# Kernel tuning notes

Hardware: AMD Instinct MI355X
Metric: run time of the kernel (lower is better)

The kernel has to match this reference:

```python
import jax, jax.numpy as jnp
import numpy as np

NODE_DIM = 256
HID = 128        # out_channels per head
HEADS = 4
NLAYERS = 2
OUT_DIM = 128
LM, LT = 30, 50
N = LM + LT       # 80 nodes per duplex graph
F = HID * HEADS   # 512
B = 1024
LN_EPS = 1e-5

def _build_edges():
    off = LM
    ms = np.arange(LM - 1); md = ms + 1
    ts = off + np.arange(LT - 1); td = ts + 1
    s1 = np.concatenate([ms, md, ts, td]); d1 = np.concatenate([md, ms, td, ts])
    ms2 = np.arange(LM - 2); md2 = ms2 + 2
    ts2 = off + np.arange(LT - 2); td2 = ts2 + 2
    s2 = np.concatenate([ms2, md2, ts2, td2]); d2 = np.concatenate([md2, ms2, td2, ts2])
    src = np.concatenate([s1, s2]).astype(np.int32)
    dst = np.concatenate([d1, d2]).astype(np.int32)
    etype = np.concatenate([np.zeros(len(s1), np.int32), np.full(len(s2), 2, np.int32)])
    return src, dst, etype

_SRC0, _DST0, _ETYPE0 = _build_edges()
E0 = len(_SRC0)                      # 308 real edges (backbone + proximity)
SRC = jnp.concatenate([jnp.asarray(_SRC0), jnp.arange(N, dtype=jnp.int32)])  # + self loops
DST = jnp.concatenate([jnp.asarray(_DST0), jnp.arange(N, dtype=jnp.int32)])
DST_BASE = jnp.asarray(_DST0)
ETYPE = jnp.asarray(_ETYPE0)

def _ln(x, g, b):
    mu = x.mean(-1, keepdims=True)
    var = ((x - mu) ** 2).mean(-1, keepdims=True)
    return (x - mu) * jax.lax.rsqrt(var + LN_EPS) * g + b

def setup_inputs() -> dict:
    key = jax.random.key(0)
    ks = jax.random.split(key, 24)
    r = lambda k, shape, fan: jax.random.normal(k, shape, jnp.float32) / np.sqrt(fan)
    inp = {
        'mirna_enc': jax.random.normal(ks[0], (B, LM, NODE_DIM), jnp.float32),
        'target_enc': jax.random.normal(ks[1], (B, LT, NODE_DIM), jnp.float32),
        'node_type_emb': r(ks[2], (2, NODE_DIM), NODE_DIM),
        'edge_type_emb': r(ks[3], (3, HEADS), HEADS),
        'in_W': r(ks[4], (NODE_DIM, F), NODE_DIM), 'in_b': jnp.zeros((F,)),
        'in_ln_g': jnp.ones((F,)), 'in_ln_b': jnp.zeros((F,)),
        'gat_Wl': r(ks[5], (NLAYERS, F, F), F), 'gat_bl': jnp.zeros((NLAYERS, F)),
        'gat_Wr': r(ks[6], (NLAYERS, F, F), F), 'gat_br': jnp.zeros((NLAYERS, F)),
        'gat_We': r(ks[7], (NLAYERS, HEADS, F), HEADS),
        'gat_att': r(ks[8], (NLAYERS, HEADS, HID), HID),
        'gat_bo': jnp.zeros((NLAYERS, F)),
        'ln_g': jnp.ones((NLAYERS, F)), 'ln_b': jnp.zeros((NLAYERS, F)),
        'out_W': r(ks[9], (2 * F, OUT_DIM), 2 * F), 'out_b': jnp.zeros((OUT_DIM,)),
        'out_ln_g': jnp.ones((OUT_DIM,)), 'out_ln_b': jnp.zeros((OUT_DIM,)),
    }
    return inp

def reference(mirna_enc, target_enc, node_type_emb, edge_type_emb, in_W, in_b,
              in_ln_g, in_ln_b, gat_Wl, gat_bl, gat_Wr, gat_br, gat_We, gat_att,
              gat_bo, ln_g, ln_b, out_W, out_b, out_ln_g, out_ln_b):
    bsz = mirna_enc.shape[0]
    x = jnp.concatenate([mirna_enc + node_type_emb[0], target_enc + node_type_emb[1]], axis=1)  # [B,N,256]
    x = jax.nn.gelu(_ln(x @ in_W + in_b, in_ln_g, in_ln_b), approximate=False)  # [B,N,F]
    # edge attributes; self-loop attr = per-dst mean of incoming edge attrs (PyG fill_value='mean')
    base = edge_type_emb[ETYPE]  # [E0, HEADS]
    cnt = jax.ops.segment_sum(jnp.ones((E0, 1), base.dtype), DST_BASE, num_segments=N)
    sl = jax.ops.segment_sum(base, DST_BASE, num_segments=N) / jnp.maximum(cnt, 1.0)
    e_attr = jnp.concatenate([base, sl], axis=0)  # [E, HEADS]
    for i in range(NLAYERS):
        ee = (e_attr @ gat_We[i]).reshape(-1, HEADS, HID)                 # [E,H,C]
        xl = (x @ gat_Wl[i] + gat_bl[i]).reshape(bsz, N, HEADS, HID)
        xr = (x @ gat_Wr[i] + gat_br[i]).reshape(bsz, N, HEADS, HID)
        att_i = gat_att[i]
        def one_graph(xl_b, xr_b):
            msg = xl_b[SRC] + xr_b[DST] + ee                              # [E,H,C]
            a = jnp.einsum('ehc,hc->eh', jax.nn.leaky_relu(msg, 0.2), att_i)
            amax = jax.ops.segment_max(a, DST, num_segments=N)            # every node has a self loop
            ex = jnp.exp(a - amax[DST])
            den = jax.ops.segment_sum(ex, DST, num_segments=N)
            alpha = ex / den[DST]                                         # [E,H]
            out = jax.ops.segment_sum(alpha[:, :, None] * xl_b[SRC], DST, num_segments=N)
            return out.reshape(N, F)
        h = jax.vmap(one_graph)(xl, xr) + gat_bo[i]
        x = _ln(h + x, ln_g[i], ln_b[i])
        if i < NLAYERS - 1:
            x = jax.nn.gelu(x, approximate=False)
    pooled = jnp.concatenate([x.mean(axis=1), x.max(axis=1)], axis=-1)    # [B, 2F]
    return jax.nn.gelu(_ln(pooled @ out_W + out_b, out_ln_g, out_ln_b), approximate=False)
```

## Files before the change

### kernel.cpp

```cpp
#include <hip/hip_runtime.h>
#include <hip/hip_bf16.h>

typedef unsigned short u16;
typedef unsigned int u32;
typedef __attribute__((ext_vector_type(8))) short bf16x8;
typedef __attribute__((ext_vector_type(4))) float f32x4;

#define NB   1024
#define LMI  30
#define LTG  50
#define NN   80
#define ROWS (NB*NN)
#define FF   512
#define HH   4
#define CC   128

__device__ __forceinline__ u16 f2b(float f) {
    u32 u = __float_as_uint(f);
    u32 r = (u + 0x7FFFu + ((u >> 16) & 1u)) >> 16;
    return (u16)r;
}
__device__ __forceinline__ float b2f(u16 h) {
    return __uint_as_float(((u32)h) << 16);
}
__device__ __forceinline__ float gelu_f(float v) {
    return 0.5f * v * (1.0f + erff(v * 0.70710678118654752440f));
}
__device__ __forceinline__ void gload_lds16(const void* g, void* l) {
    __builtin_amdgcn_global_load_lds(
        (__attribute__((address_space(1))) void*)(uintptr_t)g,
        (__attribute__((address_space(3))) void*)(uintptr_t)l,
        16, 0, 0);
}

#define X_OFF     0ULL
#define XLR_OFF   83886080ULL
#define INWT_OFF  251658240ULL
#define WLRT_OFF  (INWT_OFF + 262144ULL)
#define BIAS_OFF  (WLRT_OFF + 2097152ULL)
#define EER_OFF   (BIAS_OFF + 8192ULL)
#define EES_OFF   (EER_OFF + 8192ULL)

__global__ __launch_bounds__(256)
void prep_misc(const float* __restrict__ in_W, const float* __restrict__ gat_Wl,
               const float* __restrict__ gat_bl, const float* __restrict__ gat_Wr,
               const float* __restrict__ gat_br, const float* __restrict__ gat_We,
               const float* __restrict__ eemb,
               u16* __restrict__ inWt, u16* __restrict__ Wlrt,
               float* __restrict__ biaslr, float* __restrict__ eereal,
               float* __restrict__ eeself)
{
    int idx = blockIdx.x * 256 + threadIdx.x;
    if (idx < 131072) {
        int n = idx >> 8, k = idx & 255;
        inWt[idx] = f2b(in_W[k * 512 + n]);
        return;
    }
    idx -= 131072;
    if (idx < 1048576) {
        int l = idx >> 19; int r = idx & 524287; int n = r >> 9, k = r & 511;
        float v = (n < 512) ? gat_Wl[(size_t)l * 262144 + (size_t)k * 512 + n]
                            : gat_Wr[(size_t)l * 262144 + (size_t)k * 512 + (n - 512)];
        Wlrt[idx] = f2b(v);
        return;
    }
    idx -= 1048576;
    if (idx < 2048) {
        int l = idx >> 10, n = idx & 1023;
        biaslr[idx] = (n < 512) ? gat_bl[l * 512 + n] : gat_br[l * 512 + (n - 512)];
        return;
    }
    idx -= 2048;
    if (idx < 2048) {
        int l = idx >> 10; int r = idx & 1023; int t = r >> 9, f = r & 511;
        int et = t ? 2 : 0;
        float v = 0.f;
        #pragma unroll
        for (int h = 0; h < 4; ++h)
            v += eemb[et * 4 + h] * gat_We[l * 2048 + h * 512 + f];
        eereal[idx] = v;
        return;
    }
    idx -= 2048;
    if (idx < 81920) {
        int l = idx / 40960; int r = idx % 40960; int n = r >> 9, f = r & 511;
        int LL = (n < LMI) ? LMI : LTG;
        int p  = (n < LMI) ? n : (n - LMI);
        float c1 = (float)((p >= 1) + (p <= LL - 2));
        float c2 = (float)((p >= 2) + (p <= LL - 3));
        float ic = 1.0f / (c1 + c2);
        float v = 0.f;
        #pragma unroll
        for (int h = 0; h < 4; ++h) {
            float attr = (c1 * eemb[0 * 4 + h] + c2 * eemb[2 * 4 + h]) * ic;
            v += attr * gat_We[l * 2048 + h * 512 + f];
        }
        eeself[idx] = v;
        return;
    }
}

__global__ __launch_bounds__(256)
void prep_xin(const float* __restrict__ mirna, const float* __restrict__ target,
              const float* __restrict__ nte, u16* __restrict__ xin)
{
    int bid = blockIdx.x * 4 + (threadIdx.x >> 6);
    int b = bid / NN, n = bid % NN;
    int t = threadIdx.x & 63;
    const float* src; const float* tv;
    if (n < LMI) { src = mirna + ((size_t)b * LMI + n) * 256; tv = nte; }
    else         { src = target + ((size_t)b * LTG + (n - LMI)) * 256; tv = nte + 256; }
    float4 v = *(const float4*)(src + t * 4);
    float4 e = *(const float4*)(tv + t * 4);
    u32 p0 = (u32)f2b(v.x + e.x) | ((u32)f2b(v.y + e.y) << 16);
    u32 p1 = (u32)f2b(v.z + e.z) | ((u32)f2b(v.w + e.w) << 16);
    *(uint2*)(xin + (size_t)bid * 256 + t * 4) = make_uint2(p0, p1);
}

template<int N, int K>
__global__ __launch_bounds__(1024, 1)
void gemm_nt_bias(const u16* __restrict__ A, const u16* __restrict__ Bt,
                  const float* __restrict__ bias, u16* __restrict__ Cout)
{
    __shared__ __align__(16) u16 sm[3][2][8192];
    const int tid = threadIdx.x;
    const int w = tid >> 6, l = tid & 63;
    constexpr int ncb = N / 256;
    constexpr int nsteps = K >> 5;

    const int per = gridDim.x >> 3;
    const int nid = (blockIdx.x & 7) * per + (blockIdx.x >> 3);
    const int row0 = (nid / ncb) * 256;
    const int col0 = (nid % ncb) * 256;
    const int wr = w >> 2, wc = w & 3;

    const int srow = l >> 2;
    const int kperm = ((l & 3) ^ ((l >> 3) & 3)) * 8;
    const u16* Ag = A  + (size_t)(row0 + w * 16 + srow) * K + kperm;
    const u16* Bg = Bt + (size_t)(col0 + w * 16 + srow) * K + kperm;

#define STAGE(buf, t) do { int _ko = (t) << 5;              \
        gload_lds16(Ag + _ko, &sm[buf][0][w * 512]);        \
        gload_lds16(Bg + _ko, &sm[buf][1][w * 512]);        \
    } while (0)

    f32x4 acc[4][4];
    #pragma unroll
    for (int r = 0; r < 4; ++r)
        #pragma unroll
        for (int f = 0; f < 4; ++f)
            acc[r][f] = (f32x4){0.f, 0.f, 0.f, 0.f};

    STAGE(0, 0);
    STAGE(1, 1);

    const int ll = l & 15, lh = l >> 4;
    const int aoff = ll * 32 + ((lh ^ ((ll >> 1) & 3)) * 8);
    const int aB = wr * 4 * 512 + aoff;
    const int bB = wc * 4 * 512 + aoff;

    #pragma unroll
    for (int t = 0; t < nsteps; ++t) {
        const int cur = t % 3;
        if (t + 1 < nsteps) {
            asm volatile("s_waitcnt vmcnt(2)" ::: "memory");
        } else {
            asm volatile("s_waitcnt vmcnt(0)" ::: "memory");
        }
        __builtin_amdgcn_s_barrier();

        bf16x8 af[4], bfr[4];
        #pragma unroll
        for (int ar = 0; ar < 4; ++ar)
            af[ar] = *(const bf16x8*)&sm[cur][0][aB + ar * 512];
        #pragma unroll
        for (int fc = 0; fc < 4; ++fc)
            bfr[fc] = *(const bf16x8*)&sm[cur][1][bB + fc * 512];

        if (t + 2 < nsteps) STAGE((t + 2) % 3, t + 2);

        __builtin_amdgcn_s_setprio(1);
        #pragma unroll
        for (int ar = 0; ar < 4; ++ar)
            #pragma unroll
            for (int fc = 0; fc < 4; ++fc)
                acc[ar][fc] = __builtin_amdgcn_mfma_f32_16x16x32_bf16(
                    bfr[fc], af[ar], acc[ar][fc], 0, 0, 0);
        __builtin_amdgcn_s_setprio(0);
    }
#undef STAGE

    #pragma unroll
    for (int ar = 0; ar < 4; ++ar) {
        int grow = row0 + wr * 64 + ar * 16 + ll;
        #pragma unroll
        for (int fc = 0; fc < 4; ++fc) {
            int n0 = col0 + wc * 64 + fc * 16 + lh * 4;
            float4 bv = *(const float4*)(bias + n0);
            u32 lo = (u32)f2b(acc[ar][fc][0] + bv.x) | ((u32)f2b(acc[ar][fc][1] + bv.y) << 16);
            u32 hi = (u32)f2b(acc[ar][fc][2] + bv.z) | ((u32)f2b(acc[ar][fc][3] + bv.w) << 16);
            *(uint2*)&Cout[(size_t)grow * N + n0] = make_uint2(lo, hi);
        }
    }
}

__global__ __launch_bounds__(256)
void ln_gelu_rows(u16* __restrict__ x, const float* __restrict__ g, const float* __restrict__ b)
{
    int w = threadIdx.x >> 6, l = threadIdx.x & 63;
    size_t row = (size_t)blockIdx.x * 4 + w;
    u16* rp = x + row * FF + l * 8;
    bf16x8 v = *(const bf16x8*)rp;
    float y[8]; float s = 0.f, q = 0.f;
    #pragma unroll
    for (int j = 0; j < 8; ++j) { y[j] = b2f((u16)v[j]); s += y[j]; q += y[j] * y[j]; }
    #pragma unroll
    for (int st = 32; st; st >>= 1) { s += __shfl_xor(s, st, 64); q += __shfl_xor(q, st, 64); }
    float mu = s * (1.0f / 512.0f);
    float var = q * (1.0f / 512.0f) - mu * mu;
    float rs = rsqrtf(var + 1e-5f);
    float4 g0 = *(const float4*)(g + l * 8), g1 = *(const float4*)(g + l * 8 + 4);
    float4 b0 = *(const float4*)(b + l * 8), b1 = *(const float4*)(b + l * 8 + 4);
    float gv[8] = {g0.x, g0.y, g0.z, g0.w, g1.x, g1.y, g1.z, g1.w};
    float bv[8] = {b0.x, b0.y, b0.z, b0.w, b1.x, b1.y, b1.z, b1.w};
    bf16x8 o;
    #pragma unroll
    for (int j = 0; j < 8; ++j) {
        float z = (y[j] - mu) * rs * gv[j] + bv[j];
        o[j] = (short)f2b(gelu_f(z));
    }
    *(bf16x8*)rp = o;
}

__global__ __launch_bounds__(256)
void gat_layer(u16* __restrict__ x, const u16* __restrict__ xlr,
               const float* __restrict__ att, const float* __restrict__ eereal,
               const float* __restrict__ eeself, const float* __restrict__ bo,
               const float* __restrict__ g, const float* __restrict__ bta,
               int apply_gelu)
{
    int tid = threadIdx.x;
    int h = tid >> 6, l = tid & 63;
    int s = l >> 4, t = l & 15;
    int row = blockIdx.x * 4 + s;
    int n = row % NN;
    int lo = (n < LMI) ? 0 : LMI;
    int hi = (n < LMI) ? (LMI - 1) : (NN - 1);
    int c = h * CC + t * 8;

    bf16x8 xrv = *(const bf16x8*)(xlr + (size_t)row * 1024 + 512 + c);
    float xr[8], atv[8];
    #pragma unroll
    for (int j = 0; j < 8; ++j) xr[j] = b2f((u16)xrv[j]);
    {
        float4 a0 = *(const float4*)(att + c), a1 = *(const float4*)(att + c + 4);
        atv[0]=a0.x; atv[1]=a0.y; atv[2]=a0.z; atv[3]=a0.w;
        atv[4]=a1.x; atv[5]=a1.y; atv[6]=a1.z; atv[7]=a1.w;
    }

    bf16x8 vsave[5];
    float p5[5];
    float amax = -1e30f;
    #pragma unroll
    for (int i = 0; i < 5; ++i) {
        int d = i - 2;
        int src = n + d;
        bool ok = (src >= lo) && (src <= hi);
        int dd = ok ? d : 0;
        bf16x8 vv = *(const bf16x8*)(xlr + (size_t)(row + dd) * 1024 + c);
        vsave[i] = vv;
        const float* ee = (i == 2) ? (eeself + (size_t)n * 512 + c)
                        : ((i == 1 || i == 3) ? (eereal + c) : (eereal + 512 + c));
        float4 e0 = *(const float4*)ee, e1 = *(const float4*)(ee + 4);
        float eez[8] = {e0.x, e0.y, e0.z, e0.w, e1.x, e1.y, e1.z, e1.w};
        float p = 0.f;
        #pragma unroll
        for (int j = 0; j < 8; ++j) {
            float m = b2f((u16)vv[j]) + xr[j] + eez[j];
            m = m > 0.f ? m : 0.2f * m;
            p += m * atv[j];
        }
        p += __shfl_xor(p, 1, 64);
        p += __shfl_xor(p, 2, 64);
        p += __shfl_xor(p, 4, 64);
        p += __shfl_xor(p, 8, 64);
        p = ok ? p : -1e30f;
        p5[i] = p;
        amax = fmaxf(amax, p);
    }
    float den = 0.f;
    float o[8] = {0.f,0.f,0.f,0.f,0.f,0.f,0.f,0.f};
    #pragma unroll
    for (int i = 0; i < 5; ++i) {
        float ex = __expf(p5[i] - amax);
        den += ex;
        #pragma unroll
        for (int j = 0; j < 8; ++j) o[j] += ex * b2f((u16)vsave[i][j]);
    }
    float inv = 1.0f / den;

    u16* xrow = x + (size_t)row * FF + c;
    bf16x8 xv = *(const bf16x8*)xrow;
    float bov[8];
    {
        float4 b0 = *(const float4*)(bo + c), b1 = *(const float4*)(bo + c + 4);
        bov[0]=b0.x; bov[1]=b0.y; bov[2]=b0.z; bov[3]=b0.w;
        bov[4]=b1.x; bov[5]=b1.y; bov[6]=b1.z; bov[7]=b1.w;
    }
    float y[8]; float sum = 0.f, sq = 0.f;
    #pragma unroll
    for (int j = 0; j < 8; ++j) {
        y[j] = o[j] * inv + bov[j] + b2f((u16)xv[j]);
        sum += y[j]; sq += y[j] * y[j];
    }
    sum += __shfl_xor(sum, 1, 64); sq += __shfl_xor(sq, 1, 64);
    sum += __shfl_xor(sum, 2, 64); sq += __shfl_xor(sq, 2, 64);
    sum += __shfl_xor(sum, 4, 64); sq += __shfl_xor(sq, 4, 64);
    sum += __shfl_xor(sum, 8, 64); sq += __shfl_xor(sq, 8, 64);

    __shared__ float ssum[4][4], ssq[4][4];
    if (t == 0) { ssum[h][s] = sum; ssq[h][s] = sq; }
    __syncthreads();
    float tot = ssum[0][s] + ssum[1][s] + ssum[2][s] + ssum[3][s];
    float tq  = ssq[0][s] + ssq[1][s] + ssq[2][s] + ssq[3][s];
    float mu = tot * (1.0f / 512.0f);
    float var = tq * (1.0f / 512.0f) - mu * mu;
    float rs = rsqrtf(var + 1e-5f);

    float gv[8], btv[8];
    {
        float4 g0 = *(const float4*)(g + c), g1 = *(const float4*)(g + c + 4);
        float4 t0 = *(const float4*)(bta + c), t1 = *(const float4*)(bta + c + 4);
        gv[0]=g0.x; gv[1]=g0.y; gv[2]=g0.z; gv[3]=g0.w;
        gv[4]=g1.x; gv[5]=g1.y; gv[6]=g1.z; gv[7]=g1.w;
        btv[0]=t0.x; btv[1]=t0.y; btv[2]=t0.z; btv[3]=t0.w;
        btv[4]=t1.x; btv[5]=t1.y; btv[6]=t1.z; btv[7]=t1.w;
    }
    bf16x8 ov;
    #pragma unroll
    for (int j = 0; j < 8; ++j) {
        float z = (y[j] - mu) * rs * gv[j] + btv[j];
        if (apply_gelu) z = gelu_f(z);
        ov[j] = (short)f2b(z);
    }
    *(bf16x8*)xrow = ov;
}

__global__ __launch_bounds__(512)
void pool_kernel(const u16* __restrict__ x, u16* __restrict__ pooled)
{
    int b = blockIdx.x;
    int f = threadIdx.x;
    const u16* base = x + (size_t)b * NN * FF + f;
    float s = 0.f, mx = -1e30f;
    #pragma unroll 4
    for (int n = 0; n < NN; ++n) {
        float v = b2f(base[(size_t)n * FF]);
        s += v; mx = fmaxf(mx, v);
    }
    pooled[(size_t)b * 1024 + f]       = f2b(s * (1.0f / 80.0f));
    pooled[(size_t)b * 1024 + 512 + f] = f2b(mx);
}

__global__ __launch_bounds__(128)
void out_head(const u16* __restrict__ pooled, const float* __restrict__ W,
              const float* __restrict__ bia, const float* __restrict__ g,
              const float* __restrict__ bt, float* __restrict__ out)
{
    int b = blockIdx.x;
    int j = threadIdx.x;
    __shared__ float prow[1024];
    for (int i = j; i < 1024; i += 128) prow[i] = b2f(pooled[(size_t)b * 1024 + i]);
    __syncthreads();
    float acc = 0.f;
    #pragma unroll 8
    for (int k = 0; k < 1024; ++k) acc += prow[k] * W[k * 128 + j];
    acc += bia[j];
    float s = acc, q = acc * acc;
    #pragma unroll
    for (int st = 32; st; st >>= 1) { s += __shfl_xor(s, st, 64); q += __shfl_xor(q, st, 64); }
    __shared__ float ps[2], pq[2];
    int w = j >> 6;
    if ((j & 63) == 0) { ps[w] = s; pq[w] = q; }
    __syncthreads();
    float tot = ps[0] + ps[1], tq = pq[0] + pq[1];
    float mu = tot * (1.0f / 128.0f);
    float var = tq * (1.0f / 128.0f) - mu * mu;
    float rs = rsqrtf(var + 1e-5f);
    float z = (acc - mu) * rs * g[j] + bt[j];
    out[(size_t)b * 128 + j] = gelu_f(z);
}

extern "C" void kernel_launch(void* const* d_in, const int* in_sizes, int n_in,
                              void* d_out, int out_size, void* d_ws, size_t ws_size,
                              hipStream_t stream)
{
    (void)in_sizes; (void)n_in; (void)out_size; (void)ws_size;
    const float* mirna    = (const float*)d_in[0];
    const float* target   = (const float*)d_in[1];
    const float* nte      = (const float*)d_in[2];
    const float* eemb     = (const float*)d_in[3];
    const float* in_W     = (const float*)d_in[4];
    const float* in_b     = (const float*)d_in[5];
    const float* in_ln_g  = (const float*)d_in[6];
    const float* in_ln_b  = (const float*)d_in[7];
    const float* gat_Wl   = (const float*)d_in[8];
    const float* gat_bl   = (const float*)d_in[9];
    const float* gat_Wr   = (const float*)d_in[10];
    const float* gat_br   = (const float*)d_in[11];
    const float* gat_We   = (const float*)d_in[12];
    const float* gat_att  = (const float*)d_in[13];
    const float* gat_bo   = (const float*)d_in[14];
    const float* ln_g     = (const float*)d_in[15];
    const float* ln_b     = (const float*)d_in[16];
    const float* out_W    = (const float*)d_in[17];
    const float* out_b    = (const float*)d_in[18];
    const float* out_ln_g = (const float*)d_in[19];
    const float* out_ln_b = (const float*)d_in[20];

    char* ws = (char*)d_ws;
    u16*   x      = (u16*)(ws + X_OFF);
    u16*   xlr    = (u16*)(ws + XLR_OFF);
    u16*   xin    = xlr;
    u16*   pooled = xlr;
    u16*   inWt   = (u16*)(ws + INWT_OFF);
    u16*   Wlrt   = (u16*)(ws + WLRT_OFF);
    float* biaslr = (float*)(ws + BIAS_OFF);
    float* eereal = (float*)(ws + EER_OFF);
    float* eeself = (float*)(ws + EES_OFF);

    prep_misc<<<4944, 256, 0, stream>>>(in_W, gat_Wl, gat_bl, gat_Wr, gat_br, gat_We, eemb,
                                        inWt, Wlrt, biaslr, eereal, eeself);
    prep_xin<<<ROWS / 4, 256, 0, stream>>>(mirna, target, nte, xin);

    gemm_nt_bias<512, 256><<<(ROWS / 256) * 2, 1024, 0, stream>>>(xin, inWt, in_b, x);
    ln_gelu_rows<<<ROWS / 4, 256, 0, stream>>>(x, in_ln_g, in_ln_b);

    for (int l = 0; l < 2; ++l) {
        gemm_nt_bias<1024, 512><<<(ROWS / 256) * 4, 1024, 0, stream>>>(
            x, Wlrt + (size_t)l * 524288, biaslr + l * 1024, xlr);
        gat_layer<<<ROWS / 4, 256, 0, stream>>>(x, xlr,
                                                gat_att + l * 512,
                                                eereal + l * 1024,
                                                eeself + (size_t)l * 40960,
                                                gat_bo + l * 512,
                                                ln_g + l * 512, ln_b + l * 512,
                                                (l == 0) ? 1 : 0);
    }

    pool_kernel<<<NB, 512, 0, stream>>>(x, pooled);
    out_head<<<NB, 128, 0, stream>>>(pooled, out_W, out_b, out_ln_g, out_ln_b, (float*)d_out);
}
```

Measured before the change: 571.3 us.

## Pre-swizzle GAT weights into fragment order and load B directly to registers

The weight matrices are now rearranged during prep into the exact MFMA fragment layout, so the GEMM reads B operands straight from global memory into double-buffered registers and keeps only A staged in shared memory. Blocks shrink to 512 threads with each wave computing 128x64 instead of 64x64, which halves LDS use so two blocks can share a CU. This is meant to cut LDS traffic and barrier pressure, at the cost of more accumulator registers and B fetches that are not shared across waves. The GAT layer also precomputes xr plus the edge embeddings once and keeps the unpacked values in registers, removing repeated embedding loads.

```diff
diff --git a/kernel.cpp b/kernel.cpp
--- a/kernel.cpp
+++ b/kernel.cpp
@@ -52,13 +52,20 @@
 {
     int idx = blockIdx.x * 256 + threadIdx.x;
     if (idx < 131072) {
-        int n = idx >> 8, k = idx & 255;
+        int e = idx & 7, lane = (idx >> 3) & 63, kk = (idx >> 9) & 1;
+        int fc = (idx >> 10) & 3, kt = (idx >> 12) & 3, cg = idx >> 14;
+        int n = cg * 64 + fc * 16 + (lane & 15);
+        int k = kt * 64 + (kk * 4 + (lane >> 4)) * 8 + e;
         inWt[idx] = f2b(in_W[k * 512 + n]);
         return;
     }
     idx -= 131072;
     if (idx < 1048576) {
-        int l = idx >> 19; int r = idx & 524287; int n = r >> 9, k = r & 511;
+        int l = idx >> 19; int r = idx & 524287;
+        int e = r & 7, lane = (r >> 3) & 63, kk = (r >> 9) & 1;
+        int fc = (r >> 10) & 3, kt = (r >> 12) & 7, cg = r >> 15;
+        int n = cg * 64 + fc * 16 + (lane & 15);
+        int k = kt * 64 + (kk * 4 + (lane >> 4)) * 8 + e;
         float v = (n < 512) ? gat_Wl[(size_t)l * 262144 + (size_t)k * 512 + n]
                             : gat_Wr[(size_t)l * 262144 + (size_t)k * 512 + (n - 512)];
         Wlrt[idx] = f2b(v);
@@ -118,15 +125,16 @@
 }
 
 template<int N, int K>
-__global__ __launch_bounds__(1024, 1)
-void gemm_nt_bias(const u16* __restrict__ A, const u16* __restrict__ Bt,
+__global__ __launch_bounds__(512, 2)
+void gemm_nt_bias(const u16* __restrict__ A, const u16* __restrict__ Bf,
                   const float* __restrict__ bias, u16* __restrict__ Cout)
 {
-    __shared__ __align__(16) u16 sm[3][2][8192];
+    __shared__ __align__(16) u16 sm[3][8192];
     const int tid = threadIdx.x;
     const int w = tid >> 6, l = tid & 63;
     constexpr int ncb = N / 256;
     constexpr int nsteps = K >> 5;
+    constexpr int KT64 = K / 64;
 
     const int per = gridDim.x >> 3;
     const int nid = (blockIdx.x & 7) * per + (blockIdx.x >> 3);
@@ -136,63 +144,68 @@
 
     const int srow = l >> 2;
     const int kperm = ((l & 3) ^ ((l >> 3) & 3)) * 8;
-    const u16* Ag = A  + (size_t)(row0 + w * 16 + srow) * K + kperm;
-    const u16* Bg = Bt + (size_t)(col0 + w * 16 + srow) * K + kperm;
-
-#define STAGE(buf, t) do { int _ko = (t) << 5;              \
-        gload_lds16(Ag + _ko, &sm[buf][0][w * 512]);        \
-        gload_lds16(Bg + _ko, &sm[buf][1][w * 512]);        \
+    const u16* Ag0 = A + (size_t)(row0 + (2 * w) * 16 + srow) * K + kperm;
+    const u16* Ag1 = A + (size_t)(row0 + (2 * w + 1) * 16 + srow) * K + kperm;
+
+#define STAGE(buf, t) do { int _ko = (t) << 5;                  \
+        gload_lds16(Ag0 + _ko, &sm[buf][(2 * w) * 512]);        \
+        gload_lds16(Ag1 + _ko, &sm[buf][(2 * w + 1) * 512]);    \
     } while (0)
 
-    f32x4 acc[4][4];
-    #pragma unroll
-    for (int r = 0; r < 4; ++r)
+    const u16* Bw = Bf + (size_t)(col0 / 64 + wc) * (KT64 * 4096) + l * 8;
+
+    f32x4 acc[8][4];
+    #pragma unroll
+    for (int r = 0; r < 8; ++r)
         #pragma unroll
         for (int f = 0; f < 4; ++f)
             acc[r][f] = (f32x4){0.f, 0.f, 0.f, 0.f};
 
     STAGE(0, 0);
     STAGE(1, 1);
+    bf16x8 bfr[2][4];
+    #pragma unroll
+    for (int fc = 0; fc < 4; ++fc)
+        bfr[0][fc] = *(const bf16x8*)(Bw + (size_t)(fc * 2) * 512);
 
     const int ll = l & 15, lh = l >> 4;
     const int aoff = ll * 32 + ((lh ^ ((ll >> 1) & 3)) * 8);
-    const int aB = wr * 4 * 512 + aoff;
-    const int bB = wc * 4 * 512 + aoff;
+    const int aB = wr * 8 * 512 + aoff;
 
     #pragma unroll
     for (int t = 0; t < nsteps; ++t) {
         const int cur = t % 3;
+        asm volatile("s_waitcnt vmcnt(6)" ::: "memory");
+        __builtin_amdgcn_s_barrier();
+
+        bf16x8 af[8];
+        #pragma unroll
+        for (int ar = 0; ar < 8; ++ar)
+            af[ar] = *(const bf16x8*)&sm[cur][aB + ar * 512];
+
+        if (t + 2 < nsteps) STAGE((t + 2) % 3, t + 2);
+        asm volatile("" ::: "memory");
         if (t + 1 < nsteps) {
-            asm volatile("s_waitcnt vmcnt(2)" ::: "memory");
-        } else {
-            asm volatile("s_waitcnt vmcnt(0)" ::: "memory");
+            #pragma unroll
+            for (int fc = 0; fc < 4; ++fc)
+                bfr[(t + 1) & 1][fc] = *(const bf16x8*)
+                    (Bw + (size_t)(((t + 1) >> 1) * 8 + fc * 2 + ((t + 1) & 1)) * 512);
         }
-        __builtin_amdgcn_s_barrier();
-
-        bf16x8 af[4], bfr[4];
-        #pragma unroll
-        for (int ar = 0; ar < 4; ++ar)
-            af[ar] = *(const bf16x8*)&sm[cur][0][aB + ar * 512];
-        #pragma unroll
-        for (int fc = 0; fc < 4; ++fc)
-            bfr[fc] = *(const bf16x8*)&sm[cur][1][bB + fc * 512];
-
-        if (t + 2 < nsteps) STAGE((t + 2) % 3, t + 2);
 
         __builtin_amdgcn_s_setprio(1);
         #pragma unroll
-        for (int ar = 0; ar < 4; ++ar)
+        for (int ar = 0; ar < 8; ++ar)
             #pragma unroll
             for (int fc = 0; fc < 4; ++fc)
                 acc[ar][fc] = __builtin_amdgcn_mfma_f32_16x16x32_bf16(
-                    bfr[fc], af[ar], acc[ar][fc], 0, 0, 0);
+                    bfr[t & 1][fc], af[ar], acc[ar][fc], 0, 0, 0);
         __builtin_amdgcn_s_setprio(0);
     }
 #undef STAGE
 
     #pragma unroll
-    for (int ar = 0; ar < 4; ++ar) {
-        int grow = row0 + wr * 64 + ar * 16 + ll;
+    for (int ar = 0; ar < 8; ++ar) {
+        int grow = row0 + wr * 128 + ar * 16 + ll;
         #pragma unroll
         for (int fc = 0; fc < 4; ++fc) {
             int n0 = col0 + wc * 64 + fc * 16 + lh * 4;
@@ -258,7 +271,26 @@
         atv[4]=a1.x; atv[5]=a1.y; atv[6]=a1.z; atv[7]=a1.w;
     }
 
-    bf16x8 vsave[5];
+    float xre[3][8];
+    {
+        const float* e0p = eereal + c;
+        const float* e1p = eereal + 512 + c;
+        const float* e2p = eeself + (size_t)n * 512 + c;
+        float4 a0 = *(const float4*)e0p, a1 = *(const float4*)(e0p + 4);
+        float4 b0 = *(const float4*)e1p, b1 = *(const float4*)(e1p + 4);
+        float4 c0 = *(const float4*)e2p, c1 = *(const float4*)(e2p + 4);
+        float e0a[8] = {a0.x,a0.y,a0.z,a0.w,a1.x,a1.y,a1.z,a1.w};
+        float e1a[8] = {b0.x,b0.y,b0.z,b0.w,b1.x,b1.y,b1.z,b1.w};
+        float e2a[8] = {c0.x,c0.y,c0.z,c0.w,c1.x,c1.y,c1.z,c1.w};
+        #pragma unroll
+        for (int j = 0; j < 8; ++j) {
+            xre[0][j] = xr[j] + e0a[j];
+            xre[1][j] = xr[j] + e1a[j];
+            xre[2][j] = xr[j] + e2a[j];
+        }
+    }
+
+    float vf[5][8];
     float p5[5];
     float amax = -1e30f;
     #pragma unroll
@@ -268,16 +300,14 @@
         bool ok = (src >= lo) && (src <= hi);
         int dd = ok ? d : 0;
         bf16x8 vv = *(const bf16x8*)(xlr + (size_t)(row + dd) * 1024 + c);
-        vsave[i] = vv;
-        const float* ee = (i == 2) ? (eeself + (size_t)n * 512 + c)
-                        : ((i == 1 || i == 3) ? (eereal + c) : (eereal + 512 + c));
-        float4 e0 = *(const float4*)ee, e1 = *(const float4*)(ee + 4);
-        float eez[8] = {e0.x, e0.y, e0.z, e0.w, e1.x, e1.y, e1.z, e1.w};
+        const int sel = (i == 2) ? 2 : ((i == 1 || i == 3) ? 0 : 1);
         float p = 0.f;
         #pragma unroll
         for (int j = 0; j < 8; ++j) {
-            float m = b2f((u16)vv[j]) + xr[j] + eez[j];
-            m = m > 0.f ? m : 0.2f * m;
+            float v = b2f((u16)vv[j]);
+            vf[i][j] = v;
+            float m = v + xre[sel][j];
+            m = fmaxf(m, m * 0.2f);
             p += m * atv[j];
         }
         p += __shfl_xor(p, 1, 64);
@@ -295,7 +325,7 @@
         float ex = __expf(p5[i] - amax);
         den += ex;
         #pragma unroll
-        for (int j = 0; j < 8; ++j) o[j] += ex * b2f((u16)vsave[i][j]);
+        for (int j = 0; j < 8; ++j) o[j] += ex * vf[i][j];
     }
     float inv = 1.0f / den;
 
@@ -433,11 +463,11 @@
                                         inWt, Wlrt, biaslr, eereal, eeself);
     prep_xin<<<ROWS / 4, 256, 0, stream>>>(mirna, target, nte, xin);
 
-    gemm_nt_bias<512, 256><<<(ROWS / 256) * 2, 1024, 0, stream>>>(xin, inWt, in_b, x);
+    gemm_nt_bias<512, 256><<<(ROWS / 256) * 2, 512, 0, stream>>>(xin, inWt, in_b, x);
     ln_gelu_rows<<<ROWS / 4, 256, 0, stream>>>(x, in_ln_g, in_ln_b);
 
     for (int l = 0; l < 2; ++l) {
-        gemm_nt_bias<1024, 512><<<(ROWS / 256) * 4, 1024, 0, stream>>>(
+        gemm_nt_bias<1024, 512><<<(ROWS / 256) * 4, 512, 0, stream>>>(
             x, Wlrt + (size_t)l * 524288, biaslr + l * 1024, xlr);
         gat_layer<<<ROWS / 4, 256, 0, stream>>>(x, xlr,
                                                 gat_att + l * 512,
```

After: 567.9 us. About the same (-0.6%).

## Switch GEMM to double-buffered 64-wide K steps and precompute edge terms in attention

Applied to the files above, without the earlier changes.

The GEMM drops its triple-buffered 32-wide K pipeline for a double-buffered one. Each K step is now 64 wide and is split into two LDS sub-tiles, so there are half as many barriers and iterations. The trade-off is that the next-stage prefetch now only overlaps one step of MFMA work and needs a full vmcnt(0) wait before each barrier. Separately, the GAT attention kernel precomputes the xr+edge-embedding sums once per thread, caches the converted float values, and uses fmaxf for the leaky ReLU, which removes redundant loads and conversions inside the 5-neighbour loop.

```diff
diff --git a/kernel.cpp b/kernel.cpp
--- a/kernel.cpp
+++ b/kernel.cpp
@@ -122,11 +122,11 @@
 void gemm_nt_bias(const u16* __restrict__ A, const u16* __restrict__ Bt,
                   const float* __restrict__ bias, u16* __restrict__ Cout)
 {
-    __shared__ __align__(16) u16 sm[3][2][8192];
+    __shared__ __align__(16) u16 sm[2][4][8192];
     const int tid = threadIdx.x;
     const int w = tid >> 6, l = tid & 63;
     constexpr int ncb = N / 256;
-    constexpr int nsteps = K >> 5;
+    constexpr int nsteps = K >> 6;
 
     const int per = gridDim.x >> 3;
     const int nid = (blockIdx.x & 7) * per + (blockIdx.x >> 3);
@@ -139,9 +139,11 @@
     const u16* Ag = A  + (size_t)(row0 + w * 16 + srow) * K + kperm;
     const u16* Bg = Bt + (size_t)(col0 + w * 16 + srow) * K + kperm;
 
-#define STAGE(buf, t) do { int _ko = (t) << 5;              \
-        gload_lds16(Ag + _ko, &sm[buf][0][w * 512]);        \
-        gload_lds16(Bg + _ko, &sm[buf][1][w * 512]);        \
+#define STAGE(buf, t) do { int _ko = (t) << 6;                  \
+        gload_lds16(Ag + _ko,      &sm[buf][0][w * 512]);       \
+        gload_lds16(Ag + _ko + 32, &sm[buf][1][w * 512]);       \
+        gload_lds16(Bg + _ko,      &sm[buf][2][w * 512]);       \
+        gload_lds16(Bg + _ko + 32, &sm[buf][3][w * 512]);       \
     } while (0)
 
     f32x4 acc[4][4];
@@ -150,43 +152,44 @@
         #pragma unroll
         for (int f = 0; f < 4; ++f)
             acc[r][f] = (f32x4){0.f, 0.f, 0.f, 0.f};
-
-    STAGE(0, 0);
-    STAGE(1, 1);
 
     const int ll = l & 15, lh = l >> 4;
     const int aoff = ll * 32 + ((lh ^ ((ll >> 1) & 3)) * 8);
     const int aB = wr * 4 * 512 + aoff;
     const int bB = wc * 4 * 512 + aoff;
 
+    STAGE(0, 0);
+    asm volatile("s_waitcnt vmcnt(0)" ::: "memory");
+    __builtin_amdgcn_s_barrier();
+
     #pragma unroll
     for (int t = 0; t < nsteps; ++t) {
-        const int cur = t % 3;
-        if (t + 1 < nsteps) {
-            asm volatile("s_waitcnt vmcnt(2)" ::: "memory");
-        } else {
-            asm volatile("s_waitcnt vmcnt(0)" ::: "memory");
-        }
-        __builtin_amdgcn_s_barrier();
-
-        bf16x8 af[4], bfr[4];
-        #pragma unroll
-        for (int ar = 0; ar < 4; ++ar)
-            af[ar] = *(const bf16x8*)&sm[cur][0][aB + ar * 512];
-        #pragma unroll
-        for (int fc = 0; fc < 4; ++fc)
-            bfr[fc] = *(const bf16x8*)&sm[cur][1][bB + fc * 512];
-
-        if (t + 2 < nsteps) STAGE((t + 2) % 3, t + 2);
-
-        __builtin_amdgcn_s_setprio(1);
-        #pragma unroll
-        for (int ar = 0; ar < 4; ++ar)
+        const int cur = t & 1;
+        if (t + 1 < nsteps) STAGE(cur ^ 1, t + 1);
+
+        #pragma unroll
+        for (int kh = 0; kh < 2; ++kh) {
+            bf16x8 af[4], bfr[4];
+            #pragma unroll
+            for (int ar = 0; ar < 4; ++ar)
+                af[ar] = *(const bf16x8*)&sm[cur][kh][aB + ar * 512];
             #pragma unroll
             for (int fc = 0; fc < 4; ++fc)
-                acc[ar][fc] = __builtin_amdgcn_mfma_f32_16x16x32_bf16(
-                    bfr[fc], af[ar], acc[ar][fc], 0, 0, 0);
-        __builtin_amdgcn_s_setprio(0);
+                bfr[fc] = *(const bf16x8*)&sm[cur][2 + kh][bB + fc * 512];
+            __builtin_amdgcn_s_setprio(1);
+            #pragma unroll
+            for (int ar = 0; ar < 4; ++ar)
+                #pragma unroll
+                for (int fc = 0; fc < 4; ++fc)
+                    acc[ar][fc] = __builtin_amdgcn_mfma_f32_16x16x32_bf16(
+                        bfr[fc], af[ar], acc[ar][fc], 0, 0, 0);
+            __builtin_amdgcn_s_setprio(0);
+        }
+
+        if (t + 1 < nsteps) {
+            asm volatile("s_waitcnt vmcnt(0)" ::: "memory");
+            __builtin_amdgcn_s_barrier();
+        }
     }
 #undef STAGE
 
@@ -258,7 +261,26 @@
         atv[4]=a1.x; atv[5]=a1.y; atv[6]=a1.z; atv[7]=a1.w;
     }
 
-    bf16x8 vsave[5];
+    float xre[3][8];
+    {
+        const float* e0p = eereal + c;
+        const float* e1p = eereal + 512 + c;
+        const float* e2p = eeself + (size_t)n * 512 + c;
+        float4 a0 = *(const float4*)e0p, a1 = *(const float4*)(e0p + 4);
+        float4 b0 = *(const float4*)e1p, b1 = *(const float4*)(e1p + 4);
+        float4 c0 = *(const float4*)e2p, c1 = *(const float4*)(e2p + 4);
+        float e0a[8] = {a0.x,a0.y,a0.z,a0.w,a1.x,a1.y,a1.z,a1.w};
+        float e1a[8] = {b0.x,b0.y,b0.z,b0.w,b1.x,b1.y,b1.z,b1.w};
+        float e2a[8] = {c0.x,c0.y,c0.z,c0.w,c1.x,c1.y,c1.z,c1.w};
+        #pragma unroll
+        for (int j = 0; j < 8; ++j) {
+            xre[0][j] = xr[j] + e0a[j];
+            xre[1][j] = xr[j] + e1a[j];
+            xre[2][j] = xr[j] + e2a[j];
+        }
+    }
+
+    float vf[5][8];
     float p5[5];
     float amax = -1e30f;
     #pragma unroll
@@ -268,16 +290,14 @@
         bool ok = (src >= lo) && (src <= hi);
         int dd = ok ? d : 0;
         bf16x8 vv = *(const bf16x8*)(xlr + (size_t)(row + dd) * 1024 + c);
-        vsave[i] = vv;
-        const float* ee = (i == 2) ? (eeself + (size_t)n * 512 + c)
-                        : ((i == 1 || i == 3) ? (eereal + c) : (eereal + 512 + c));
-        float4 e0 = *(const float4*)ee, e1 = *(const float4*)(ee + 4);
-        float eez[8] = {e0.x, e0.y, e0.z, e0.w, e1.x, e1.y, e1.z, e1.w};
+        const int sel = (i == 2) ? 2 : ((i == 1 || i == 3) ? 0 : 1);
         float p = 0.f;
         #pragma unroll
         for (int j = 0; j < 8; ++j) {
-            float m = b2f((u16)vv[j]) + xr[j] + eez[j];
-            m = m > 0.f ? m : 0.2f * m;
+            float v = b2f((u16)vv[j]);
+            vf[i][j] = v;
+            float m = v + xre[sel][j];
+            m = fmaxf(m, m * 0.2f);
             p += m * atv[j];
         }
         p += __shfl_xor(p, 1, 64);
@@ -295,7 +315,7 @@
         float ex = __expf(p5[i] - amax);
         den += ex;
         #pragma unroll
-        for (int j = 0; j < 8; ++j) o[j] += ex * b2f((u16)vsave[i][j]);
+        for (int j = 0; j < 8; ++j) o[j] += ex * vf[i][j];
     }
     float inv = 1.0f / den;
 
```

New measurement: 544.5 us (median of 2 runs). 1.05x faster.
